# Optimization experiments

Hardware: AMD Instinct MI355X
Metric: run time of the kernel (lower is better)

Reference implementation:

```python
import jax, jax.numpy as jnp
import numpy as np
from jax import lax

EPS_IN = 1e-5  # torch InstanceNorm1d eps


def instance_norm(x, w, b):
    # x: (B, C, T); normalize over T per (B, C), biased variance
    mu = x.mean(axis=-1, keepdims=True)
    var = x.var(axis=-1, keepdims=True)
    return (x - mu) * lax.rsqrt(var + EPS_IN) * w[None, :, None] + b[None, :, None]


def conv1x1(x, w):
    # w: (O, I, 1)
    return jnp.einsum('oi,bit->bot', w[:, :, 0], x)


def setup_inputs() -> dict:
    key = jax.random.key(0)
    ks = jax.random.split(key, 16)
    B, C, T, NC = 32, 64, 2048, 4
    enc_dim = C * 3 * 4
    d = {
        'xb': jax.random.normal(ks[0], (B, 3, C, T), jnp.float32),
        'mu': jnp.linspace(-3.0, 3.0, 4),
        'sigma': jnp.full((4,), 2.0),
        'sconv1_w': jax.random.normal(ks[1], (128, enc_dim, 1)) * (1.0 / np.sqrt(enc_dim)),
        'in1_w': 1.0 + 0.1 * jax.random.normal(ks[2], (128,)),
        'in1_b': 0.1 * jax.random.normal(ks[3], (128,)),
        'sconv2_w': jax.random.normal(ks[4], (C, 128, 1)) * (1.0 / np.sqrt(128)),
        'in2_w': 1.0 + 0.1 * jax.random.normal(ks[5], (C,)),
        'in2_b': 0.1 * jax.random.normal(ks[6], (C,)),
        'tconv1_w': jax.random.normal(ks[7], (C, C, 15)) * (1.0 / np.sqrt(C * 15)),
        'in3_w': 1.0 + 0.1 * jax.random.normal(ks[8], (C,)),
        'in3_b': 0.1 * jax.random.normal(ks[9], (C,)),
        'tconv2_w': jax.random.normal(ks[10], (C, C, 1)) * (1.0 / np.sqrt(C)),
        'in4_w': 1.0 + 0.1 * jax.random.normal(ks[11], (C,)),
        'in4_b': 0.1 * jax.random.normal(ks[12], (C,)),
        'alpha': jnp.asarray(0.5),
        'gamma': jnp.asarray(0.5),
        'beta_logit': jnp.asarray(1.0),
        'fc_w': jax.random.normal(ks[13], (4, C)) * (1.0 / np.sqrt(C)),
        'fc_b': 0.1 * jax.random.normal(ks[14], (4,)),
    }
    return d


def reference(xb, mu, sigma, sconv1_w, in1_w, in1_b, sconv2_w, in2_w, in2_b,
              tconv1_w, in3_w, in3_b, tconv2_w, in4_w, in4_b,
              alpha, gamma, beta_logit, fc_w, fc_b):
    B, Ftypes, C, T = xb.shape
    V_BASE = 1.0
    Tp = T // 8

    # pooled curvature / tangent streams -> (T', B, C)
    curv_p = xb[:, 1].reshape(B, C, Tp, 8).mean(-1).transpose(2, 0, 1)
    tang_p = xb[:, 2].reshape(B, C, Tp, 8).mean(-1).transpose(2, 0, 1)

    # learnable population encoding: (B,3,C,T,4) -> (B, 3*C*4, T)
    enc = jnp.exp(-(xb[..., None] - mu) ** 2 / (2.0 * sigma ** 2 + 1e-6))
    x_enc = enc.transpose(0, 1, 2, 4, 3).reshape(B, Ftypes * C * 4, T)

    # spatial 1x1 convs + instance norm + relu
    h = jax.nn.relu(instance_norm(conv1x1(x_enc, sconv1_w), in1_w, in1_b))
    h = jax.nn.relu(instance_norm(conv1x1(h, sconv2_w), in2_w, in2_b))

    # temporal conv k=15 pad=7, 1x1 conv, avg pool 8
    h = lax.conv_general_dilated(h, tconv1_w, (1,), [(7, 7)],
                                 dimension_numbers=('NCH', 'OIH', 'NCH'))
    h = jax.nn.relu(instance_norm(h, in3_w, in3_b))
    h = jax.nn.relu(instance_norm(conv1x1(h, tconv2_w), in4_w, in4_b))
    h = h.reshape(B, C, Tp, 8).mean(-1)  # AvgPool1d(8)
    # dropout is identity in eval mode
    c = h.transpose(2, 0, 1)  # (T', B, C)

    # sequential GD-LIF recurrence over T' steps
    def step(m, inp):
        x_t, curv_t, tang_t = inp
        v_th = V_BASE + alpha * tang_t
        beta = jax.nn.sigmoid(beta_logit - gamma * curv_t)
        m_next = beta * m + x_t
        spike = (m_next - v_th > 0).astype(m_next.dtype)
        m_next = m_next - spike * v_th
        return m_next, spike

    m0 = jnp.zeros((B, C), xb.dtype)
    _, spikes = lax.scan(step, m0, (c, curv_p, tang_p))  # (T', B, C)

    attn = jax.nn.softmax(curv_p, axis=0)
    out_feat = jnp.sum(spikes * attn, axis=0)  # (B, C)
    return out_feat @ fc_w.T + fc_b
```

## Files before the change

### kernel.cpp

```cpp
#include <hip/hip_runtime.h>
#include <math.h>

#define TLEN 2048
#define TP 256

typedef double d4 __attribute__((ext_vector_type(4)));

__device__ __forceinline__ double block_reduce_sum_d(double v, double* sm) {
#pragma unroll
  for (int off = 32; off > 0; off >>= 1) v += __shfl_down(v, off, 64);
  int lane = threadIdx.x & 63, wid = threadIdx.x >> 6;
  __syncthreads();
  if (lane == 0) sm[wid] = v;
  __syncthreads();
  double r = sm[0] + sm[1] + sm[2] + sm[3];
  __syncthreads();
  return r;
}

__global__ void k_probe_f64(int* __restrict__ tbl) {
  int l = threadIdx.x;
  __shared__ int kaS[64], kbS[64];
  __shared__ int cnt[256];
  int rdv[4] = {-1, -1, -1, -1}, cdv[4] = {-1, -1, -1, -1};
  int mav = -1, nbv = -1;
  int okr = 1;
  int nrow = 0, ncol = 0;
  kaS[l] = -1; kbS[l] = -1;
  __syncthreads();

  for (int j = 0; j < 64; ++j) {
    double a = (l == j) ? 1.0 : 0.0;
    d4 acc = {0.0, 0.0, 0.0, 0.0};
    acc = __builtin_amdgcn_mfma_f64_16x16x4f64(a, 1.0, acc, 0, 0, 0);
    int mylab = -1;
#pragma unroll
    for (int v = 0; v < 4; ++v) if (acc[v] != 0.0 && rdv[v] >= 0) mylab = rdv[v];
#pragma unroll
    for (int off = 32; off >= 1; off >>= 1) {
      int o = __shfl_xor(mylab, off);
      mylab = mylab > o ? mylab : o;
    }
    int label = (mylab < 0) ? nrow : mylab;
    if (mylab < 0) nrow++;
    if (label >= 16) okr = 0;
#pragma unroll
    for (int v = 0; v < 4; ++v) if (acc[v] != 0.0) rdv[v] = label;
    if (l == j) mav = label;
  }

  for (int j = 0; j < 64; ++j) {
    double bb = (l == j) ? 1.0 : 0.0;
    d4 acc = {0.0, 0.0, 0.0, 0.0};
    acc = __builtin_amdgcn_mfma_f64_16x16x4f64(1.0, bb, acc, 0, 0, 0);
    int mylab = -1;
#pragma unroll
    for (int v = 0; v < 4; ++v) if (acc[v] != 0.0 && cdv[v] >= 0) mylab = cdv[v];
#pragma unroll
    for (int off = 32; off >= 1; off >>= 1) {
      int o = __shfl_xor(mylab, off);
      mylab = mylab > o ? mylab : o;
    }
    int label = (mylab < 0) ? ncol : mylab;
    if (mylab < 0) ncol++;
    if (label >= 16) okr = 0;
#pragma unroll
    for (int v = 0; v < 4; ++v) if (acc[v] != 0.0) cdv[v] = label;
    if (l == j) nbv = label;
  }

  unsigned long long row0 = __ballot(mav == 0);
  if (__popcll(row0) != 4) okr = 0;
  for (int i = 0; i < 4; ++i) {
    int rep = -1, idx = -1;
    for (int t = 0; t < 64; ++t)
      if ((row0 >> t) & 1ull) { if (++idx == i) { rep = t; break; } }
    double a = (l == rep) ? 1.0 : 0.0;
    double bb = (double)(l + 1);
    d4 acc = {0.0, 0.0, 0.0, 0.0};
    acc = __builtin_amdgcn_mfma_f64_16x16x4f64(a, bb, acc, 0, 0, 0);
#pragma unroll
    for (int v = 0; v < 4; ++v)
      if (rdv[v] == 0) {
        int jp = (int)(acc[v] + 0.5) - 1;
        if (jp >= 0 && jp < 64) kbS[jp] = i; else okr = 0;
      }
  }
  __syncthreads();
  int kbv = kbS[l];

  for (int i = 0; i < 4; ++i) {
    unsigned long long bm = __ballot(kbv == i);
    int rep = -1;
    if (bm != 0ull) { rep = 0; while (!((bm >> rep) & 1ull)) ++rep; }
    else okr = 0;
    int nc = (rep >= 0) ? __shfl(nbv, rep) : -2;
    double bb = (l == rep) ? 1.0 : 0.0;
    double aa = (double)(l + 1);
    d4 acc = {0.0, 0.0, 0.0, 0.0};
    acc = __builtin_amdgcn_mfma_f64_16x16x4f64(aa, bb, acc, 0, 0, 0);
#pragma unroll
    for (int v = 0; v < 4; ++v)
      if (cdv[v] == nc) {
        int jp = (int)(acc[v] + 0.5) - 1;
        if (jp >= 0 && jp < 64) kaS[jp] = i; else okr = 0;
      }
  }
  __syncthreads();
  int kav = kaS[l];

  if (nrow != 16 || ncol != 16) okr = 0;
  if (mav < 0 || mav > 15 || nbv < 0 || nbv > 15 ||
      kav < 0 || kav > 3 || kbv < 0 || kbv > 3) okr = 0;
#pragma unroll
  for (int v = 0; v < 4; ++v)
    if (rdv[v] < 0 || rdv[v] > 15 || cdv[v] < 0 || cdv[v] > 15) okr = 0;
  cnt[l] = 0; cnt[64 + l] = 0; cnt[128 + l] = 0; cnt[192 + l] = 0;
  __syncthreads();
  if (mav >= 0 && mav < 16 && kav >= 0 && kav < 4) atomicAdd(&cnt[mav * 4 + kav], 1);
  if (kbv >= 0 && kbv < 4 && nbv >= 0 && nbv < 16) atomicAdd(&cnt[64 + kbv * 16 + nbv], 1);
  __syncthreads();
  if (cnt[l] != 1 || cnt[64 + l] != 1) okr = 0;
  __syncthreads();
  cnt[l] = 0; cnt[64 + l] = 0; cnt[128 + l] = 0; cnt[192 + l] = 0;
  __syncthreads();
#pragma unroll
  for (int v = 0; v < 4; ++v)
    if (rdv[v] >= 0 && rdv[v] < 16 && cdv[v] >= 0 && cdv[v] < 16)
      atomicAdd(&cnt[rdv[v] * 16 + cdv[v]], 1);
  __syncthreads();
#pragma unroll
  for (int v = 0; v < 4; ++v) if (cnt[l * 4 + v] != 1) okr = 0;
  if (mav == 0) {
    int rank = (int)__popcll(row0 & ((1ull << l) - 1ull));
    if (kav != rank) okr = 0;
  }
  unsigned long long good = __ballot(okr != 0);
  tbl[l] = mav; tbl[64 + l] = kav; tbl[128 + l] = kbv; tbl[192 + l] = nbv;
#pragma unroll
  for (int v = 0; v < 4; ++v) {
    tbl[256 + l * 4 + v] = rdv[v];
    tbl[512 + l * 4 + v] = cdv[v];
  }
  if (l == 0) tbl[768] = (good == 0xFFFFFFFFFFFFFFFFull) ? 1 : 0;
}

__global__ void k_repack_w(const float* __restrict__ w, float* __restrict__ wT) {
  int idx = blockIdx.x * 256 + threadIdx.x;
  if (idx >= 64 * 64 * 15) return;
  int o = idx & 63, i = (idx >> 6) & 63, k = idx >> 12;
  wT[idx] = w[(o * 64 + i) * 15 + k];
}

template <typename T>
__global__ __launch_bounds__(256) void k_pool_ct(const float* __restrict__ xb,
                                                 T* __restrict__ curvp,
                                                 T* __restrict__ tangp) {
  int row = blockIdx.x;
  int b = row >> 6, c = row & 63;
  int tid = threadIdx.x;
  const float* s1 = xb + ((size_t)((b * 3 + 1) * 64 + c)) * TLEN + tid * 8;
  const float* s2 = xb + ((size_t)((b * 3 + 2) * 64 + c)) * TLEN + tid * 8;
  double p1 = 0.0, p2 = 0.0;
#pragma unroll
  for (int j = 0; j < 8; ++j) { p1 += (double)s1[j]; p2 += (double)s2[j]; }
  curvp[(size_t)row * TP + tid] = (T)(p1 * 0.125);
  tangp[(size_t)row * TP + tid] = (T)(p2 * 0.125);
}

template <typename T>
__global__ __launch_bounds__(256) void k_stats(const T* __restrict__ h,
                                               const float* __restrict__ gw,
                                               const float* __restrict__ gb,
                                               int chmask,
                                               double* __restrict__ sc,
                                               double* __restrict__ sh) {
  __shared__ double sm[4];
  int row = blockIdx.x, tid = threadIdx.x;
  int ch = row & chmask;
  const T* base = h + (size_t)row * TLEN + tid * 8;
  double v[8];
#pragma unroll
  for (int j = 0; j < 8; ++j) v[j] = (double)base[j];
  double s = 0.0;
#pragma unroll
  for (int j = 0; j < 8; ++j) s += v[j];
  double mean = block_reduce_sum_d(s, sm) * (1.0 / 2048.0);
  double sq = 0.0;
#pragma unroll
  for (int j = 0; j < 8; ++j) { double d = v[j] - mean; sq += d * d; }
  double var = block_reduce_sum_d(sq, sm) * (1.0 / 2048.0);
  double scale = (double)gw[ch] / sqrt(var + 1e-5);
  double shift = (double)gb[ch] - mean * scale;
  if (tid == 0) { sc[row] = scale; sh[row] = shift; }
}

template <typename T>
__global__ __launch_bounds__(512, 4) void k_enc1_mfma(const float* __restrict__ xb,
                                                      const float* __restrict__ w,
                                                      const float* __restrict__ mu,
                                                      const float* __restrict__ sigma,
                                                      T* __restrict__ h1,
                                                      const int* __restrict__ tbl) {
  if (tbl[768] == 0) return;
  __shared__ float AsT[32][132];
  __shared__ double Bs[32][132];
  __shared__ double smu[4], sinv[4];
  int b = blockIdx.x, t0 = blockIdx.y * 128, tid = threadIdx.x;
  int wv = tid >> 6, l = tid & 63;
  int o0 = (wv >> 1) * 32, tb = (wv & 1) * 64;
  int t_ma = tbl[l], t_ka = tbl[64 + l], t_kb = tbl[128 + l], t_nb = tbl[192 + l];
  int t_rd[4], t_cd[4];
#pragma unroll
  for (int v = 0; v < 4; ++v) { t_rd[v] = tbl[256 + l * 4 + v]; t_cd[v] = tbl[512 + l * 4 + v]; }
  if (tid < 4) {
    smu[tid] = (double)mu[tid];
    double s = (double)sigma[tid];
    sinv[tid] = 1.0 / (2.0 * s * s + 1e-6);
  }
  d4 acc[2][4];
#pragma unroll
  for (int r = 0; r < 2; ++r)
#pragma unroll
    for (int c = 0; c < 4; ++c) acc[r][c] = (d4){0.0, 0.0, 0.0, 0.0};

  for (int kc = 0; kc < 24; ++kc) {
    int i0 = kc * 32;
    __syncthreads();
    {
      int idx = tid * 4;
#pragma unroll
      for (int rep = 0; rep < 2; ++rep) {
        int o = idx >> 5, ii = idx & 31;
        float4 v4 = *(const float4*)(w + (size_t)o * 768 + i0 + ii);
        AsT[ii][o] = v4.x; AsT[ii + 1][o] = v4.y; AsT[ii + 2][o] = v4.z; AsT[ii + 3][o] = v4.w;
        idx += 2048;
      }
    }
    {
      int f = i0 >> 8;
      int cb = (i0 >> 2) & 63;
      int c = tid >> 6, l2 = tid & 63;
      int t = 2 * l2;
      float2 x2 = *(const float2*)(xb + ((size_t)((b * 3 + f) * 64 + cb + c)) * TLEN + t0 + t);
      double xv0 = (double)x2.x, xv1 = (double)x2.y;
#pragma unroll
      for (int g = 0; g < 4; ++g) {
        double m = smu[g], inv = sinv[g];
        double d0 = xv0 - m, d1 = xv1 - m;
        double2 e = {exp(-d0 * d0 * inv), exp(-d1 * d1 * inv)};
        *(double2*)&Bs[c * 4 + g][t] = e;
      }
    }
    __syncthreads();
#pragma unroll
    for (int k4 = 0; k4 < 32; k4 += 4) {
      double aF0 = (double)AsT[k4 + t_ka][o0 + t_ma];
      double aF1 = (double)AsT[k4 + t_ka][o0 + 16 + t_ma];
      double bF[4];
#pragma unroll
      for (int c = 0; c < 4; ++c) bF[c] = Bs[k4 + t_kb][tb + c * 16 + t_nb];
#pragma unroll
      for (int c = 0; c < 4; ++c) {
        acc[0][c] = __builtin_amdgcn_mfma_f64_16x16x4f64(aF0, bF[c], acc[0][c], 0, 0, 0);
        acc[1][c] = __builtin_amdgcn_mfma_f64_16x16x4f64(aF1, bF[c], acc[1][c], 0, 0, 0);
      }
    }
  }
#pragma unroll
  for (int r = 0; r < 2; ++r)
#pragma unroll
    for (int c = 0; c < 4; ++c)
#pragma unroll
      for (int v = 0; v < 4; ++v) {
        int o = o0 + r * 16 + t_rd[v];
        h1[((size_t)(b * 128 + o)) * TLEN + t0 + tb + c * 16 + t_cd[v]] = (T)acc[r][c][v];
      }
}

template <typename T>
__global__ __launch_bounds__(256, 4) void k_enc1_valu(const float* __restrict__ xb,
                                                      const float* __restrict__ w,
                                                      const float* __restrict__ mu,
                                                      const float* __restrict__ sigma,
                                                      T* __restrict__ h1,
                                                      const int* __restrict__ tbl) {
  if (tbl[768] != 0) return;
  __shared__ float AsT[32][132];
  __shared__ double Bs[32][64];
  __shared__ double smu[4], sinv[4];
  int b = blockIdx.x, t0 = blockIdx.y * 64, tid = threadIdx.x;
  if (tid < 4) {
    smu[tid] = (double)mu[tid];
    double s = (double)sigma[tid];
    sinv[tid] = 1.0 / (2.0 * s * s + 1e-6);
  }
  double acc[8][4] = {};
  int to = (tid >> 4) * 8, l = tid & 15;
  for (int kc = 0; kc < 24; ++kc) {
    int i0 = kc * 32;
    __syncthreads();
    {
      int idx = tid * 4;
#pragma unroll
      for (int rep = 0; rep < 4; ++rep) {
        int o = idx >> 5, ii = idx & 31;
        float4 v4 = *(const float4*)(w + (size_t)o * 768 + i0 + ii);
        AsT[ii][o] = v4.x; AsT[ii + 1][o] = v4.y; AsT[ii + 2][o] = v4.z; AsT[ii + 3][o] = v4.w;
        idx += 1024;
      }
    }
    {
      int f = i0 >> 8;
      int cb = (i0 >> 2) & 63;
      int c = tid >> 5, l2 = tid & 31;
      int t = 2 * l2;
      float2 x2 = *(const float2*)(xb + ((size_t)((b * 3 + f) * 64 + cb + c)) * TLEN + t0 + t);
      double xv0 = (double)x2.x, xv1 = (double)x2.y;
#pragma unroll
      for (int g = 0; g < 4; ++g) {
        double m = smu[g], inv = sinv[g];
        double d0 = xv0 - m, d1 = xv1 - m;
        double2 e = {exp(-d0 * d0 * inv), exp(-d1 * d1 * inv)};
        *(double2*)&Bs[c * 4 + g][t] = e;
      }
    }
    __syncthreads();
#pragma unroll
    for (int kk = 0; kk < 32; ++kk) {
      float4 a0 = *(const float4*)&AsT[kk][to];
      float4 a1 = *(const float4*)&AsT[kk][to + 4];
      double a[8] = {(double)a0.x, (double)a0.y, (double)a0.z, (double)a0.w,
                     (double)a1.x, (double)a1.y, (double)a1.z, (double)a1.w};
      double bb[4];
#pragma unroll
      for (int j = 0; j < 2; ++j) {
        double2 p = *(const double2*)&Bs[kk][2 * l + 32 * j];
        bb[2 * j] = p.x; bb[2 * j + 1] = p.y;
      }
#pragma unroll
      for (int q = 0; q < 8; ++q)
#pragma unroll
        for (int j = 0; j < 4; ++j) acc[q][j] += a[q] * bb[j];
    }
  }
#pragma unroll
  for (int q = 0; q < 8; ++q) {
    T* op = h1 + ((size_t)(b * 128 + to + q)) * TLEN + t0;
    op[2 * l]      = (T)acc[q][0];
    op[2 * l + 1]  = (T)acc[q][1];
    op[2 * l + 32] = (T)acc[q][2];
    op[2 * l + 33] = (T)acc[q][3];
  }
}

template <int K, typename T>
__global__ __launch_bounds__(256, 4) void k_conv1x1_mfma(const T* __restrict__ in,
                                                         const float* __restrict__ w,
                                                         const double* __restrict__ sc,
                                                         const double* __restrict__ sh,
                                                         T* __restrict__ out,
                                                         const int* __restrict__ tbl) {
  if (tbl[768] == 0) return;
  __shared__ float AsT[32][68];
  __shared__ double Bs[32][68];
  int b = blockIdx.x, t0 = blockIdx.y * 64, tid = threadIdx.x;
  int wv = tid >> 6, l = tid & 63;
  int t_ma = tbl[l], t_ka = tbl[64 + l], t_kb = tbl[128 + l], t_nb = tbl[192 + l];
  int t_rd[4], t_cd[4];
#pragma unroll
  for (int v = 0; v < 4; ++v) { t_rd[v] = tbl[256 + l * 4 + v]; t_cd[v] = tbl[512 + l * 4 + v]; }
  int o0 = wv * 16;
  d4 acc[4];
#pragma unroll
  for (int c = 0; c < 4; ++c) acc[c] = (d4){0.0, 0.0, 0.0, 0.0};
  for (int kc = 0; kc < K / 32; ++kc) {
    __syncthreads();
    {
      int idx = tid * 4;
#pragma unroll
      for (int rep = 0; rep < 2; ++rep) {
        int o = idx >> 5, ii = idx & 31;
        float4 v4 = *(const float4*)(w + (size_t)o * K + kc * 32 + ii);
        AsT[ii][o] = v4.x; AsT[ii + 1][o] = v4.y; AsT[ii + 2][o] = v4.z; AsT[ii + 3][o] = v4.w;
        idx += 1024;
      }
    }
    {
      int r = tid >> 3, l8 = tid & 7;
      int srow = b * K + kc * 32 + r;
      const T* gp = in + (size_t)srow * TLEN + t0;
      double s_ = sc[srow], h_ = sh[srow];
#pragma unroll
      for (int q = 0; q < 4; ++q) {
        int t = 2 * l8 + 16 * q;
        double2 v = {fmax((double)gp[t] * s_ + h_, 0.0),
                     fmax((double)gp[t + 1] * s_ + h_, 0.0)};
        *(double2*)&Bs[r][t] = v;
      }
    }
    __syncthreads();
#pragma unroll
    for (int k4 = 0; k4 < 32; k4 += 4) {
      double aF = (double)AsT[k4 + t_ka][o0 + t_ma];
#pragma unroll
      for (int c = 0; c < 4; ++c) {
        double bF = Bs[k4 + t_kb][c * 16 + t_nb];
        acc[c] = __builtin_amdgcn_mfma_f64_16x16x4f64(aF, bF, acc[c], 0, 0, 0);
      }
    }
  }
#pragma unroll
  for (int c = 0; c < 4; ++c)
#pragma unroll
    for (int v = 0; v < 4; ++v)
      out[((size_t)(b * 64 + o0 + t_rd[v])) * TLEN + t0 + c * 16 + t_cd[v]] = (T)acc[c][v];
}

template <int K, typename T>
__global__ __launch_bounds__(256, 4) void k_conv1x1_valu(const T* __restrict__ in,
                                                         const float* __restrict__ w,
                                                         const double* __restrict__ sc,
                                                         const double* __restrict__ sh,
                                                         T* __restrict__ out,
                                                         const int* __restrict__ tbl) {
  if (tbl[768] != 0) return;
  __shared__ float AsT[32][68];
  __shared__ double Bs[32][64];
  int b = blockIdx.x, t0 = blockIdx.y * 64, tid = threadIdx.x;
  double acc[4][4] = {};
  int to = (tid >> 4) * 4, l = tid & 15;
  for (int kc = 0; kc < K / 32; ++kc) {
    __syncthreads();
    {
      int idx = tid * 4;
#pragma unroll
      for (int rep = 0; rep < 2; ++rep) {
        int o = idx >> 5, ii = idx & 31;
        float4 v4 = *(const float4*)(w + (size_t)o * K + kc * 32 + ii);
        AsT[ii][o] = v4.x; AsT[ii + 1][o] = v4.y; AsT[ii + 2][o] = v4.z; AsT[ii + 3][o] = v4.w;
        idx += 1024;
      }
    }
    {
      int r = tid >> 3, l8 = tid & 7;
      int srow = b * K + kc * 32 + r;
      const T* gp = in + (size_t)srow * TLEN + t0;
      double s_ = sc[srow], h_ = sh[srow];
#pragma unroll
      for (int q = 0; q < 4; ++q) {
        int t = 2 * l8 + 16 * q;
        double2 v = {fmax((double)gp[t] * s_ + h_, 0.0),
                     fmax((double)gp[t + 1] * s_ + h_, 0.0)};
        *(double2*)&Bs[r][t] = v;
      }
    }
    __syncthreads();
#pragma unroll
    for (int kk = 0; kk < 32; ++kk) {
      float4 a4 = *(const float4*)&AsT[kk][to];
      double a0 = (double)a4.x, a1 = (double)a4.y, a2 = (double)a4.z, a3 = (double)a4.w;
      double bb[4];
#pragma unroll
      for (int j = 0; j < 2; ++j) {
        double2 p = *(const double2*)&Bs[kk][2 * l + 32 * j];
        bb[2 * j] = p.x; bb[2 * j + 1] = p.y;
      }
#pragma unroll
      for (int j = 0; j < 4; ++j) {
        acc[0][j] += a0 * bb[j];
        acc[1][j] += a1 * bb[j];
        acc[2][j] += a2 * bb[j];
        acc[3][j] += a3 * bb[j];
      }
    }
  }
#pragma unroll
  for (int q = 0; q < 4; ++q) {
    T* op = out + ((size_t)(b * 64 + to + q)) * TLEN + t0;
    op[2 * l]      = (T)acc[q][0];
    op[2 * l + 1]  = (T)acc[q][1];
    op[2 * l + 32] = (T)acc[q][2];
    op[2 * l + 33] = (T)acc[q][3];
  }
}

template <typename T>
__global__ __launch_bounds__(512, 2) void k_tconv1_mfma(const T* __restrict__ h2,
                                                        const float* __restrict__ wT,
                                                        const double* __restrict__ sc,
                                                        const double* __restrict__ sh,
                                                        T* __restrict__ h3,
                                                        const int* __restrict__ tbl) {
  if (tbl[768] == 0) return;
  __shared__ __align__(16) double In[64][80];
  __shared__ float Ws[8][15][64];
  int b = blockIdx.x, t0 = blockIdx.y * 64, tid = threadIdx.x;
  int wv = tid >> 6, l = tid & 63;
  int t_ma = tbl[l], t_ka = tbl[64 + l], t_kb = tbl[128 + l], t_nb = tbl[192 + l];
  int t_rd[4], t_cd[4];
#pragma unroll
  for (int v = 0; v < 4; ++v) { t_rd[v] = tbl[256 + l * 4 + v]; t_cd[v] = tbl[512 + l * 4 + v]; }
  int o0 = (wv >> 1) * 16, tq = (wv & 1) * 32;
  for (int idx = tid; idx < 64 * 78; idx += 512) {
    int i = idx / 78, x = idx - i * 78;
    int tg = t0 - 7 + x;
    int row = b * 64 + i;
    double v = 0.0;
    if (tg >= 0 && tg < TLEN)
      v = fmax((double)h2[(size_t)row * TLEN + tg] * sc[row] + sh[row], 0.0);
    In[i][x] = v;
  }
  d4 acc[2];
  acc[0] = (d4){0.0, 0.0, 0.0, 0.0};
  acc[1] = (d4){0.0, 0.0, 0.0, 0.0};
  for (int ic = 0; ic < 8; ++ic) {
    __syncthreads();
    for (int idx = tid; idx < 15 * 8 * 16; idx += 512) {
      int k = idx >> 7;
      int r = idx & 127;
      int ii = r >> 4, o4 = (r & 15) * 4;
      float4 v = *(const float4*)(wT + ((size_t)(k * 64 + ic * 8 + ii)) * 64 + o4);
      *(float4*)&Ws[ii][k][o4] = v;
    }
    __syncthreads();
#pragma unroll
    for (int k = 0; k < 15; ++k) {
#pragma unroll
      for (int kg = 0; kg < 2; ++kg) {
        double aF = (double)Ws[kg * 4 + t_ka][k][o0 + t_ma];
#pragma unroll
        for (int c = 0; c < 2; ++c) {
          double bF = In[ic * 8 + kg * 4 + t_kb][tq + c * 16 + t_nb + k];
          acc[c] = __builtin_amdgcn_mfma_f64_16x16x4f64(aF, bF, acc[c], 0, 0, 0);
        }
      }
    }
  }
#pragma unroll
  for (int c = 0; c < 2; ++c)
#pragma unroll
    for (int v = 0; v < 4; ++v)
      h3[((size_t)(b * 64 + o0 + t_rd[v])) * TLEN + t0 + tq + c * 16 + t_cd[v]] = (T)acc[c][v];
}

template <typename T>
__global__ __launch_bounds__(256) void k_tconv1_valu(const T* __restrict__ h2,
                                                     const float* __restrict__ wT,
                                                     const double* __restrict__ sc,
                                                     const double* __restrict__ sh,
                                                     T* __restrict__ h3,
                                                     const int* __restrict__ tbl) {
  if (tbl[768] != 0) return;
  __shared__ __align__(16) double In[64][80];
  __shared__ float Ws[8][15][64];
  int b = blockIdx.x, t0 = blockIdx.y * 64, tid = threadIdx.x;
  for (int idx = tid; idx < 64 * 78; idx += 256) {
    int i = idx / 78, x = idx - i * 78;
    int tg = t0 - 7 + x;
    int row = b * 64 + i;
    double v = 0.0;
    if (tg >= 0 && tg < TLEN)
      v = fmax((double)h2[(size_t)row * TLEN + tg] * sc[row] + sh[row], 0.0);
    In[i][x] = v;
  }
  double acc[4][4] = {};
  int og = (tid >> 4) * 4, tt2 = (tid & 15) * 4;
  for (int ic = 0; ic < 8; ++ic) {
    __syncthreads();
    for (int idx = tid; idx < 15 * 8 * 16; idx += 256) {
      int k = idx >> 7;
      int r = idx & 127;
      int ii = r >> 4, o4 = (r & 15) * 4;
      float4 v = *(const float4*)(wT + ((size_t)(k * 64 + ic * 8 + ii)) * 64 + o4);
      *(float4*)&Ws[ii][k][o4] = v;
    }
    __syncthreads();
#pragma unroll
    for (int ii = 0; ii < 8; ++ii) {
      int i = ic * 8 + ii;
      double r[18];
#pragma unroll
      for (int m = 0; m < 18; m += 2) {
        double2 p = *(const double2*)&In[i][tt2 + m];
        r[m] = p.x; r[m + 1] = p.y;
      }
#pragma unroll
      for (int k = 0; k < 15; ++k) {
        float4 w4 = *(const float4*)&Ws[ii][k][og];
        double w0 = (double)w4.x, w1 = (double)w4.y, w2 = (double)w4.z, w3 = (double)w4.w;
#pragma unroll
        for (int j = 0; j < 4; ++j) {
          double x = r[j + k];
          acc[0][j] += w0 * x;
          acc[1][j] += w1 * x;
          acc[2][j] += w2 * x;
          acc[3][j] += w3 * x;
        }
      }
    }
  }
#pragma unroll
  for (int q = 0; q < 4; ++q) {
    T* op = h3 + ((size_t)(b * 64 + og + q)) * TLEN + t0 + tt2;
#pragma unroll
    for (int j = 0; j < 4; ++j) op[j] = (T)acc[q][j];
  }
}

template <typename T>
__global__ __launch_bounds__(256) void k_in4_pool(const T* __restrict__ h,
                                                  const float* __restrict__ gw,
                                                  const float* __restrict__ gb,
                                                  T* __restrict__ cbuf) {
  __shared__ double sm[4];
  int row = blockIdx.x, tid = threadIdx.x;
  int ch = row & 63;
  const T* base = h + (size_t)row * TLEN + tid * 8;
  double v[8];
#pragma unroll
  for (int j = 0; j < 8; ++j) v[j] = (double)base[j];
  double s = 0.0;
#pragma unroll
  for (int j = 0; j < 8; ++j) s += v[j];
  double mean = block_reduce_sum_d(s, sm) * (1.0 / 2048.0);
  double sq = 0.0;
#pragma unroll
  for (int j = 0; j < 8; ++j) { double d = v[j] - mean; sq += d * d; }
  double var = block_reduce_sum_d(sq, sm) * (1.0 / 2048.0);
  double scale = (double)gw[ch] / sqrt(var + 1e-5);
  double shift = (double)gb[ch] - mean * scale;
  double p = 0.0;
#pragma unroll
  for (int j = 0; j < 8; ++j) p += fmax(v[j] * scale + shift, 0.0);
  cbuf[(size_t)row * TP + tid] = (T)(p * 0.125);
}

template <typename T>
__global__ __launch_bounds__(64) void k_scan(const T* __restrict__ cbuf,
                                             const T* __restrict__ curvp,
                                             const T* __restrict__ tangp,
                                             const float* __restrict__ alpha,
                                             const float* __restrict__ gamma,
                                             const float* __restrict__ betal,
                                             double* __restrict__ ofeat) {
  int id = blockIdx.x * 64 + threadIdx.x;
  double a = (double)alpha[0], g = (double)gamma[0], bl = (double)betal[0];
  const T* cu_p = curvp + (size_t)id * TP;
  const T* ta_p = tangp + (size_t)id * TP;
  const T* cb_p = cbuf + (size_t)id * TP;
  double mmax = -1e300, ssum = 0.0, accs = 0.0, mem = 0.0;
  for (int tp = 0; tp < TP; ++tp) {
    double cu = (double)cu_p[tp];
    double ta = (double)ta_p[tp];
    double x = (double)cb_p[tp];
    double nm = fmax(mmax, cu);
    double r = exp(mmax - nm);
    double e = exp(cu - nm);
    ssum = ssum * r + e;
    accs = accs * r;
    mmax = nm;
    double vth = 1.0 + a * ta;
    double beta = 1.0 / (1.0 + exp(g * cu - bl));
    mem = beta * mem + x;
    if (mem - vth > 0.0) {
      accs += e;
      mem -= vth;
    }
  }
  ofeat[id] = accs / ssum;
}

__global__ void k_fc(const double* __restrict__ ofeat, const float* __restrict__ fw,
                     const float* __restrict__ fb, float* __restrict__ out) {
  int tid = threadIdx.x;
  if (tid >= 128) return;
  int b = tid >> 2, j = tid & 3;
  double s = (double)fb[j];
#pragma unroll
  for (int c = 0; c < 64; ++c) s += ofeat[b * 64 + c] * (double)fw[j * 64 + c];
  out[b * 4 + j] = (float)s;
}

template <typename T>
static void run_all(void* const* d_in, float* out, char* wsb, hipStream_t stream) {
  const float* xb    = (const float*)d_in[0];
  const float* mu    = (const float*)d_in[1];
  const float* sigma = (const float*)d_in[2];
  const float* w1    = (const float*)d_in[3];
  const float* in1w  = (const float*)d_in[4];
  const float* in1b  = (const float*)d_in[5];
  const float* w2    = (const float*)d_in[6];
  const float* in2w  = (const float*)d_in[7];
  const float* in2b  = (const float*)d_in[8];
  const float* wt1   = (const float*)d_in[9];
  const float* in3w  = (const float*)d_in[10];
  const float* in3b  = (const float*)d_in[11];
  const float* w4    = (const float*)d_in[12];
  const float* in4w  = (const float*)d_in[13];
  const float* in4b  = (const float*)d_in[14];
  const float* alpha = (const float*)d_in[15];
  const float* gamma = (const float*)d_in[16];
  const float* betal = (const float*)d_in[17];
  const float* fcw   = (const float*)d_in[18];
  const float* fcb   = (const float*)d_in[19];

  size_t sT = sizeof(T);
  T* h1 = (T*)wsb;
  T* h2 = (T*)(wsb + (size_t)8388608 * sT);
  T* h3 = h1;
  T* h4 = h2;
  float* wT = (float*)(wsb + (size_t)12582912 * sT);
  char* p = wsb + (size_t)12582912 * sT + 245760;
  T* curvp = (T*)p;
  T* tangp = (T*)(p + (size_t)524288 * sT);
  T* cbuf  = (T*)(p + (size_t)2 * 524288 * sT);
  double* ofeat = (double*)(p + (size_t)3 * 524288 * sT);
  char* cb = (char*)cbuf;
  int* tbl = (int*)cb;
  double* sc1 = (double*)(cb + 16384);
  double* sh1 = sc1 + 4096;
  double* sc2 = sh1 + 4096;
  double* sh2 = sc2 + 2048;
  double* sc3 = sh2 + 2048;
  double* sh3 = sc3 + 2048;

  k_repack_w<<<dim3(240), dim3(256), 0, stream>>>(wt1, wT);
  k_pool_ct<T><<<dim3(2048), dim3(256), 0, stream>>>(xb, curvp, tangp);
  k_probe_f64<<<dim3(1), dim3(64), 0, stream>>>(tbl);
  k_enc1_mfma<T><<<dim3(32, 16), dim3(512), 0, stream>>>(xb, w1, mu, sigma, h1, tbl);
  k_enc1_valu<T><<<dim3(32, 32), dim3(256), 0, stream>>>(xb, w1, mu, sigma, h1, tbl);
  k_stats<T><<<dim3(4096), dim3(256), 0, stream>>>(h1, in1w, in1b, 127, sc1, sh1);
  k_conv1x1_mfma<128, T><<<dim3(32, 32), dim3(256), 0, stream>>>(h1, w2, sc1, sh1, h2, tbl);
  k_conv1x1_valu<128, T><<<dim3(32, 32), dim3(256), 0, stream>>>(h1, w2, sc1, sh1, h2, tbl);
  k_stats<T><<<dim3(2048), dim3(256), 0, stream>>>(h2, in2w, in2b, 63, sc2, sh2);
  k_tconv1_mfma<T><<<dim3(32, 32), dim3(512), 0, stream>>>(h2, wT, sc2, sh2, h3, tbl);
  k_tconv1_valu<T><<<dim3(32, 32), dim3(256), 0, stream>>>(h2, wT, sc2, sh2, h3, tbl);
  k_stats<T><<<dim3(2048), dim3(256), 0, stream>>>(h3, in3w, in3b, 63, sc3, sh3);
  k_conv1x1_mfma<64, T><<<dim3(32, 32), dim3(256), 0, stream>>>(h3, w4, sc3, sh3, h4, tbl);
  k_conv1x1_valu<64, T><<<dim3(32, 32), dim3(256), 0, stream>>>(h3, w4, sc3, sh3, h4, tbl);
  k_in4_pool<T><<<dim3(2048), dim3(256), 0, stream>>>(h4, in4w, in4b, cbuf);
  k_scan<T><<<dim3(32), dim3(64), 0, stream>>>(cbuf, curvp, tangp, alpha, gamma, betal, ofeat);
  k_fc<<<dim3(1), dim3(128), 0, stream>>>(ofeat, fcw, fcb, out);
}

extern "C" void kernel_launch(void* const* d_in, const int* in_sizes, int n_in,
                              void* d_out, int out_size, void* d_ws, size_t ws_size,
                              hipStream_t stream) {
  const size_t NEED64 = 113508352ull;
  if (ws_size >= NEED64)
    run_all<double>(d_in, (float*)d_out, (char*)d_ws, stream);
  else
    run_all<float>(d_in, (float*)d_out, (char*)d_ws, stream);
}
```

Baseline: 608.0 us.

## Load MFMA weight fragments directly from global memory instead of LDS staging

In the encoder, 1x1-conv and temporal-conv MFMA kernels, the weight tiles are no longer staged through shared memory. Each lane now reads its A-fragment straight from global memory, relying on L1/L2 caching since the weights are small and shared by all blocks. The encoder kernel is also reshaped from 512-thread, 128-wide time tiles to 256-thread, 64-wide tiles, which doubles the grid. This cuts LDS traffic and removes barriers in tconv1, but each MFMA step now waits on uncoalesced scalar global loads.

Result: slower. 635.8 us (+4.6%).

```diff
diff --git a/kernel.cpp b/kernel.cpp
--- a/kernel.cpp
+++ b/kernel.cpp
@@ -196,23 +196,24 @@
 }
 
 template <typename T>
-__global__ __launch_bounds__(512, 4) void k_enc1_mfma(const float* __restrict__ xb,
+__global__ __launch_bounds__(256, 4) void k_enc1_mfma(const float* __restrict__ xb,
                                                       const float* __restrict__ w,
                                                       const float* __restrict__ mu,
                                                       const float* __restrict__ sigma,
                                                       T* __restrict__ h1,
                                                       const int* __restrict__ tbl) {
   if (tbl[768] == 0) return;
-  __shared__ float AsT[32][132];
-  __shared__ double Bs[32][132];
+  __shared__ double Bs[32][68];
   __shared__ double smu[4], sinv[4];
-  int b = blockIdx.x, t0 = blockIdx.y * 128, tid = threadIdx.x;
+  int b = blockIdx.x, t0 = blockIdx.y * 64, tid = threadIdx.x;
   int wv = tid >> 6, l = tid & 63;
-  int o0 = (wv >> 1) * 32, tb = (wv & 1) * 64;
   int t_ma = tbl[l], t_ka = tbl[64 + l], t_kb = tbl[128 + l], t_nb = tbl[192 + l];
   int t_rd[4], t_cd[4];
 #pragma unroll
   for (int v = 0; v < 4; ++v) { t_rd[v] = tbl[256 + l * 4 + v]; t_cd[v] = tbl[512 + l * 4 + v]; }
+  int o0 = wv * 32;
+  const float* wA0 = w + (size_t)(o0 + t_ma) * 768 + t_ka;
+  const float* wA1 = w + (size_t)(o0 + 16 + t_ma) * 768 + t_ka;
   if (tid < 4) {
     smu[tid] = (double)mu[tid];
     double s = (double)sigma[tid];
@@ -228,19 +229,9 @@
     int i0 = kc * 32;
     __syncthreads();
     {
-      int idx = tid * 4;
-#pragma unroll
-      for (int rep = 0; rep < 2; ++rep) {
-        int o = idx >> 5, ii = idx & 31;
-        float4 v4 = *(const float4*)(w + (size_t)o * 768 + i0 + ii);
-        AsT[ii][o] = v4.x; AsT[ii + 1][o] = v4.y; AsT[ii + 2][o] = v4.z; AsT[ii + 3][o] = v4.w;
-        idx += 2048;
-      }
-    }
-    {
       int f = i0 >> 8;
       int cb = (i0 >> 2) & 63;
-      int c = tid >> 6, l2 = tid & 63;
+      int c = tid >> 5, l2 = tid & 31;
       int t = 2 * l2;
       float2 x2 = *(const float2*)(xb + ((size_t)((b * 3 + f) * 64 + cb + c)) * TLEN + t0 + t);
       double xv0 = (double)x2.x, xv1 = (double)x2.y;
@@ -255,11 +246,11 @@
     __syncthreads();
 #pragma unroll
     for (int k4 = 0; k4 < 32; k4 += 4) {
-      double aF0 = (double)AsT[k4 + t_ka][o0 + t_ma];
-      double aF1 = (double)AsT[k4 + t_ka][o0 + 16 + t_ma];
+      double aF0 = (double)wA0[i0 + k4];
+      double aF1 = (double)wA1[i0 + k4];
       double bF[4];
 #pragma unroll
-      for (int c = 0; c < 4; ++c) bF[c] = Bs[k4 + t_kb][tb + c * 16 + t_nb];
+      for (int c = 0; c < 4; ++c) bF[c] = Bs[k4 + t_kb][c * 16 + t_nb];
 #pragma unroll
       for (int c = 0; c < 4; ++c) {
         acc[0][c] = __builtin_amdgcn_mfma_f64_16x16x4f64(aF0, bF[c], acc[0][c], 0, 0, 0);
@@ -274,7 +265,7 @@
 #pragma unroll
       for (int v = 0; v < 4; ++v) {
         int o = o0 + r * 16 + t_rd[v];
-        h1[((size_t)(b * 128 + o)) * TLEN + t0 + tb + c * 16 + t_cd[v]] = (T)acc[r][c][v];
+        h1[((size_t)(b * 128 + o)) * TLEN + t0 + c * 16 + t_cd[v]] = (T)acc[r][c][v];
       }
 }
 
@@ -362,7 +353,6 @@
                                                          T* __restrict__ out,
                                                          const int* __restrict__ tbl) {
   if (tbl[768] == 0) return;
-  __shared__ float AsT[32][68];
   __shared__ double Bs[32][68];
   int b = blockIdx.x, t0 = blockIdx.y * 64, tid = threadIdx.x;
   int wv = tid >> 6, l = tid & 63;
@@ -371,21 +361,12 @@
 #pragma unroll
   for (int v = 0; v < 4; ++v) { t_rd[v] = tbl[256 + l * 4 + v]; t_cd[v] = tbl[512 + l * 4 + v]; }
   int o0 = wv * 16;
+  const float* wA = w + (size_t)(o0 + t_ma) * K + t_ka;
   d4 acc[4];
 #pragma unroll
   for (int c = 0; c < 4; ++c) acc[c] = (d4){0.0, 0.0, 0.0, 0.0};
   for (int kc = 0; kc < K / 32; ++kc) {
     __syncthreads();
-    {
-      int idx = tid * 4;
-#pragma unroll
-      for (int rep = 0; rep < 2; ++rep) {
-        int o = idx >> 5, ii = idx & 31;
-        float4 v4 = *(const float4*)(w + (size_t)o * K + kc * 32 + ii);
-        AsT[ii][o] = v4.x; AsT[ii + 1][o] = v4.y; AsT[ii + 2][o] = v4.z; AsT[ii + 3][o] = v4.w;
-        idx += 1024;
-      }
-    }
     {
       int r = tid >> 3, l8 = tid & 7;
       int srow = b * K + kc * 32 + r;
@@ -402,7 +383,7 @@
     __syncthreads();
 #pragma unroll
     for (int k4 = 0; k4 < 32; k4 += 4) {
-      double aF = (double)AsT[k4 + t_ka][o0 + t_ma];
+      double aF = (double)wA[kc * 32 + k4];
 #pragma unroll
       for (int c = 0; c < 4; ++c) {
         double bF = Bs[k4 + t_kb][c * 16 + t_nb];
@@ -494,7 +475,6 @@
                                                         const int* __restrict__ tbl) {
   if (tbl[768] == 0) return;
   __shared__ __align__(16) double In[64][80];
-  __shared__ float Ws[8][15][64];
   int b = blockIdx.x, t0 = blockIdx.y * 64, tid = threadIdx.x;
   int wv = tid >> 6, l = tid & 63;
   int t_ma = tbl[l], t_ka = tbl[64 + l], t_kb = tbl[128 + l], t_nb = tbl[192 + l];
@@ -502,6 +482,7 @@
 #pragma unroll
   for (int v = 0; v < 4; ++v) { t_rd[v] = tbl[256 + l * 4 + v]; t_cd[v] = tbl[512 + l * 4 + v]; }
   int o0 = (wv >> 1) * 16, tq = (wv & 1) * 32;
+  const float* wAp = wT + (size_t)t_ka * 64 + o0 + t_ma;
   for (int idx = tid; idx < 64 * 78; idx += 512) {
     int i = idx / 78, x = idx - i * 78;
     int tg = t0 - 7 + x;
@@ -511,24 +492,16 @@
       v = fmax((double)h2[(size_t)row * TLEN + tg] * sc[row] + sh[row], 0.0);
     In[i][x] = v;
   }
+  __syncthreads();
   d4 acc[2];
   acc[0] = (d4){0.0, 0.0, 0.0, 0.0};
   acc[1] = (d4){0.0, 0.0, 0.0, 0.0};
   for (int ic = 0; ic < 8; ++ic) {
-    __syncthreads();
-    for (int idx = tid; idx < 15 * 8 * 16; idx += 512) {
-      int k = idx >> 7;
-      int r = idx & 127;
-      int ii = r >> 4, o4 = (r & 15) * 4;
-      float4 v = *(const float4*)(wT + ((size_t)(k * 64 + ic * 8 + ii)) * 64 + o4);
-      *(float4*)&Ws[ii][k][o4] = v;
-    }
-    __syncthreads();
 #pragma unroll
     for (int k = 0; k < 15; ++k) {
 #pragma unroll
       for (int kg = 0; kg < 2; ++kg) {
-        double aF = (double)Ws[kg * 4 + t_ka][k][o0 + t_ma];
+        double aF = (double)wAp[(size_t)(k * 64 + ic * 8 + kg * 4) * 64];
 #pragma unroll
         for (int c = 0; c < 2; ++c) {
           double bF = In[ic * 8 + kg * 4 + t_kb][tq + c * 16 + t_nb + k];
@@ -728,7 +701,7 @@
   k_repack_w<<<dim3(240), dim3(256), 0, stream>>>(wt1, wT);
   k_pool_ct<T><<<dim3(2048), dim3(256), 0, stream>>>(xb, curvp, tangp);
   k_probe_f64<<<dim3(1), dim3(64), 0, stream>>>(tbl);
-  k_enc1_mfma<T><<<dim3(32, 16), dim3(512), 0, stream>>>(xb, w1, mu, sigma, h1, tbl);
+  k_enc1_mfma<T><<<dim3(32, 32), dim3(256), 0, stream>>>(xb, w1, mu, sigma, h1, tbl);
   k_enc1_valu<T><<<dim3(32, 32), dim3(256), 0, stream>>>(xb, w1, mu, sigma, h1, tbl);
   k_stats<T><<<dim3(4096), dim3(256), 0, stream>>>(h1, in1w, in1b, 127, sc1, sh1);
   k_conv1x1_mfma<128, T><<<dim3(32, 32), dim3(256), 0, stream>>>(h1, w2, sc1, sh1, h2, tbl);
```

## Prefetch next K-chunk in enc1 MFMA; read tconv1 weights directly from global

Applied to the files above, without the earlier changes.

In the enc1 MFMA kernel, the weight float4 loads and the Gaussian encoding exps for the next K chunk are computed into registers while the current chunk's MFMAs run, and the per-group mu/sigma constants move from shared memory to registers. This software pipelining is meant to hide global-load and exp latency behind the matrix work. In the tconv1 MFMA kernel, the shared-memory weight staging and its two barriers per input-channel chunk are removed, and A fragments are loaded straight from global or cache. The cost is higher register pressure in enc1 and many small uncoalesced global loads in tconv1.

New measurement: 594.5 us. -2.2%, faster.

```diff
diff --git a/kernel.cpp b/kernel.cpp
--- a/kernel.cpp
+++ b/kernel.cpp
@@ -205,7 +205,6 @@
   if (tbl[768] == 0) return;
   __shared__ float AsT[32][132];
   __shared__ double Bs[32][132];
-  __shared__ double smu[4], sinv[4];
   int b = blockIdx.x, t0 = blockIdx.y * 128, tid = threadIdx.x;
   int wv = tid >> 6, l = tid & 63;
   int o0 = (wv >> 1) * 32, tb = (wv & 1) * 64;
@@ -213,10 +212,12 @@
   int t_rd[4], t_cd[4];
 #pragma unroll
   for (int v = 0; v < 4; ++v) { t_rd[v] = tbl[256 + l * 4 + v]; t_cd[v] = tbl[512 + l * 4 + v]; }
-  if (tid < 4) {
-    smu[tid] = (double)mu[tid];
-    double s = (double)sigma[tid];
-    sinv[tid] = 1.0 / (2.0 * s * s + 1e-6);
+  double smu[4], sinv[4];
+#pragma unroll
+  for (int g = 0; g < 4; ++g) {
+    smu[g] = (double)mu[g];
+    double s = (double)sigma[g];
+    sinv[g] = 1.0 / (2.0 * s * s + 1e-6);
   }
   d4 acc[2][4];
 #pragma unroll
@@ -224,33 +225,35 @@
 #pragma unroll
     for (int c = 0; c < 4; ++c) acc[r][c] = (d4){0.0, 0.0, 0.0, 0.0};
 
+  int aO1 = (tid * 4) >> 5, aI1 = (tid * 4) & 31;
+  int aO2 = (tid * 4 + 2048) >> 5, aI2 = (tid * 4 + 2048) & 31;
+  int sc_ = tid >> 6, sl2 = tid & 63;
+  int st = 2 * sl2;
+
+  float4 a1r = *(const float4*)(w + (size_t)aO1 * 768 + aI1);
+  float4 a2r = *(const float4*)(w + (size_t)aO2 * 768 + aI2);
+  double e[8];
+  {
+    float2 x2 = *(const float2*)(xb + ((size_t)((b * 3 + 0) * 64 + 0 + sc_)) * TLEN + t0 + st);
+    double xv0 = (double)x2.x, xv1 = (double)x2.y;
+#pragma unroll
+    for (int g = 0; g < 4; ++g) {
+      double d0 = xv0 - smu[g], d1 = xv1 - smu[g];
+      e[2 * g] = exp(-d0 * d0 * sinv[g]);
+      e[2 * g + 1] = exp(-d1 * d1 * sinv[g]);
+    }
+  }
+
   for (int kc = 0; kc < 24; ++kc) {
-    int i0 = kc * 32;
-    __syncthreads();
-    {
-      int idx = tid * 4;
-#pragma unroll
-      for (int rep = 0; rep < 2; ++rep) {
-        int o = idx >> 5, ii = idx & 31;
-        float4 v4 = *(const float4*)(w + (size_t)o * 768 + i0 + ii);
-        AsT[ii][o] = v4.x; AsT[ii + 1][o] = v4.y; AsT[ii + 2][o] = v4.z; AsT[ii + 3][o] = v4.w;
-        idx += 2048;
-      }
-    }
-    {
-      int f = i0 >> 8;
-      int cb = (i0 >> 2) & 63;
-      int c = tid >> 6, l2 = tid & 63;
-      int t = 2 * l2;
-      float2 x2 = *(const float2*)(xb + ((size_t)((b * 3 + f) * 64 + cb + c)) * TLEN + t0 + t);
-      double xv0 = (double)x2.x, xv1 = (double)x2.y;
-#pragma unroll
-      for (int g = 0; g < 4; ++g) {
-        double m = smu[g], inv = sinv[g];
-        double d0 = xv0 - m, d1 = xv1 - m;
-        double2 e = {exp(-d0 * d0 * inv), exp(-d1 * d1 * inv)};
-        *(double2*)&Bs[c * 4 + g][t] = e;
-      }
+    __syncthreads();
+    AsT[aI1][aO1] = a1r.x; AsT[aI1 + 1][aO1] = a1r.y;
+    AsT[aI1 + 2][aO1] = a1r.z; AsT[aI1 + 3][aO1] = a1r.w;
+    AsT[aI2][aO2] = a2r.x; AsT[aI2 + 1][aO2] = a2r.y;
+    AsT[aI2 + 2][aO2] = a2r.z; AsT[aI2 + 3][aO2] = a2r.w;
+#pragma unroll
+    for (int g = 0; g < 4; ++g) {
+      double2 ev = {e[2 * g], e[2 * g + 1]};
+      *(double2*)&Bs[sc_ * 4 + g][st] = ev;
     }
     __syncthreads();
 #pragma unroll
@@ -264,6 +267,21 @@
       for (int c = 0; c < 4; ++c) {
         acc[0][c] = __builtin_amdgcn_mfma_f64_16x16x4f64(aF0, bF[c], acc[0][c], 0, 0, 0);
         acc[1][c] = __builtin_amdgcn_mfma_f64_16x16x4f64(aF1, bF[c], acc[1][c], 0, 0, 0);
+      }
+    }
+    if (kc < 23) {
+      int i0n = (kc + 1) * 32;
+      a1r = *(const float4*)(w + (size_t)aO1 * 768 + i0n + aI1);
+      a2r = *(const float4*)(w + (size_t)aO2 * 768 + i0n + aI2);
+      int f = i0n >> 8;
+      int cb = (i0n >> 2) & 63;
+      float2 x2 = *(const float2*)(xb + ((size_t)((b * 3 + f) * 64 + cb + sc_)) * TLEN + t0 + st);
+      double xv0 = (double)x2.x, xv1 = (double)x2.y;
+#pragma unroll
+      for (int g = 0; g < 4; ++g) {
+        double d0 = xv0 - smu[g], d1 = xv1 - smu[g];
+        e[2 * g] = exp(-d0 * d0 * sinv[g]);
+        e[2 * g + 1] = exp(-d1 * d1 * sinv[g]);
       }
     }
   }
@@ -494,7 +512,6 @@
                                                         const int* __restrict__ tbl) {
   if (tbl[768] == 0) return;
   __shared__ __align__(16) double In[64][80];
-  __shared__ float Ws[8][15][64];
   int b = blockIdx.x, t0 = blockIdx.y * 64, tid = threadIdx.x;
   int wv = tid >> 6, l = tid & 63;
   int t_ma = tbl[l], t_ka = tbl[64 + l], t_kb = tbl[128 + l], t_nb = tbl[192 + l];
@@ -502,6 +519,7 @@
 #pragma unroll
   for (int v = 0; v < 4; ++v) { t_rd[v] = tbl[256 + l * 4 + v]; t_cd[v] = tbl[512 + l * 4 + v]; }
   int o0 = (wv >> 1) * 16, tq = (wv & 1) * 32;
+  const float* wAp = wT + (size_t)t_ka * 64 + o0 + t_ma;
   for (int idx = tid; idx < 64 * 78; idx += 512) {
     int i = idx / 78, x = idx - i * 78;
     int tg = t0 - 7 + x;
@@ -511,24 +529,16 @@
       v = fmax((double)h2[(size_t)row * TLEN + tg] * sc[row] + sh[row], 0.0);
     In[i][x] = v;
   }
+  __syncthreads();
   d4 acc[2];
   acc[0] = (d4){0.0, 0.0, 0.0, 0.0};
   acc[1] = (d4){0.0, 0.0, 0.0, 0.0};
   for (int ic = 0; ic < 8; ++ic) {
-    __syncthreads();
-    for (int idx = tid; idx < 15 * 8 * 16; idx += 512) {
-      int k = idx >> 7;
-      int r = idx & 127;
-      int ii = r >> 4, o4 = (r & 15) * 4;
-      float4 v = *(const float4*)(wT + ((size_t)(k * 64 + ic * 8 + ii)) * 64 + o4);
-      *(float4*)&Ws[ii][k][o4] = v;
-    }
-    __syncthreads();
 #pragma unroll
     for (int k = 0; k < 15; ++k) {
 #pragma unroll
       for (int kg = 0; kg < 2; ++kg) {
-        double aF = (double)Ws[kg * 4 + t_ka][k][o0 + t_ma];
+        double aF = (double)wAp[(size_t)(k * 64 + ic * 8 + kg * 4) * 64];
 #pragma unroll
         for (int c = 0; c < 2; ++c) {
           double bF = In[ic * 8 + kg * 4 + t_kb][tq + c * 16 + t_nb + k];
```
